# Kernel optimization log

Hardware: AMD Instinct MI355X
Metric: run time of the kernel (lower is better)

The kernel has to match this reference:

```python
import jax, jax.numpy as jnp
import numpy as np

VOCAB, EMBED, MAXLEN, UNITS, F1, BATCH = 50000, 256, 512, 32, 16, 512

def setup_inputs() -> dict:
    key = jax.random.key(0)
    ks = jax.random.split(key, 9)
    tokens = jax.random.randint(ks[0], (BATCH, MAXLEN), 0, VOCAB, dtype=jnp.int32)
    emb_table = jax.random.normal(ks[1], (VOCAB, EMBED), dtype=jnp.float32) * 0.02
    # SimpleRNN params (Keras: kernel, recurrent_kernel, bias)
    Wx = jax.random.normal(ks[2], (EMBED, UNITS), dtype=jnp.float32) * (1.0 / np.sqrt(EMBED))
    Wh = jax.random.normal(ks[3], (UNITS, UNITS), dtype=jnp.float32) * (1.0 / np.sqrt(UNITS))
    b  = jnp.zeros((UNITS,), dtype=jnp.float32)
    W1 = jax.random.normal(ks[4], (UNITS, F1), dtype=jnp.float32) * (1.0 / np.sqrt(UNITS))
    b1 = jnp.zeros((F1,), dtype=jnp.float32)
    W2 = jax.random.normal(ks[5], (F1, 1), dtype=jnp.float32) * (1.0 / np.sqrt(F1))
    b2 = jnp.zeros((1,), dtype=jnp.float32)
    return {"tokens": tokens, "emb_table": emb_table, "Wx": Wx, "Wh": Wh, "b": b,
            "W1": W1, "b1": b1, "W2": W2, "b2": b2}

def reference(tokens, emb_table, Wx, Wh, b, W1, b1, W2, b2):
    # Embedding lookup: [B, T, E]
    x = emb_table[tokens]
    # SimpleRNN recurrence (tanh), return last hidden state. Dropout disabled (inference).
    xs = jnp.transpose(x, (1, 0, 2))  # time-major [T, B, E]
    h0 = jnp.zeros((tokens.shape[0], Wh.shape[0]), dtype=x.dtype)

    def step(h, x_t):
        h_new = jnp.tanh(x_t @ Wx + h @ Wh + b)
        return h_new, None

    h_last, _ = jax.lax.scan(step, h0, xs)
    # Flatten is a no-op on [B, 32]; Dense heads are linear (no activation), then sigmoid.
    z = (h_last @ W1 + b1) @ W2 + b2
    return jax.nn.sigmoid(z)  # [B, 1]
```

## Files before the change

### kernel.cpp

```cpp
#include <hip/hip_runtime.h>
#include <hip/hip_bf16.h>
#include <math.h>

#define TT 512
#define BB 512
#define EE 256
#define UU 32
#define FF1 16
#define NWAVE 2048

#define TWO_LOG2E 2.8853900817779268f

__device__ __forceinline__ float rdlane(float v, int lane) {
    return __int_as_float(__builtin_amdgcn_readlane(__float_as_int(v), lane));
}

#define DPP_ADD(v, ctrl)                                                    \
    (v) += __int_as_float(__builtin_amdgcn_update_dpp(                      \
        0, __float_as_int(v), (ctrl), 0xf, 0xf, true))

__global__ __launch_bounds__(64) void proj_dpp(
    const float* __restrict__ emb, const float* __restrict__ Wx,
    const float* __restrict__ bias, float* __restrict__ P, int nrows)
{
    const int L = threadIdx.x;
    const int g = L >> 4;
    const int c = L & 15;
    const int wv = blockIdx.x;

    float w[16][8];
    #pragma unroll
    for (int kk = 0; kk < 16; ++kk) {
        const float4* src = (const float4*)(Wx + (size_t)(kk * 16 + c) * UU + g * 8);
        float4 a = src[0], b = src[1];
        w[kk][0] = a.x; w[kk][1] = a.y; w[kk][2] = a.z; w[kk][3] = a.w;
        w[kk][4] = b.x; w[kk][5] = b.y; w[kk][6] = b.z; w[kk][7] = b.w;
    }
    float bs[8];
    #pragma unroll
    for (int uu = 0; uu < 8; ++uu) bs[uu] = bias[g * 8 + uu];

    auto rowptr = [&](int i) {
        int r = wv + NWAVE * i;
        if (r >= nrows) r = nrows - 1;
        return emb + (size_t)r * EE;
    };

    float xA[16], xB[16];
    {
        const float* rp = rowptr(0);
        #pragma unroll
        for (int kk = 0; kk < 16; ++kk) xA[kk] = rp[kk * 16 + c];
    }

    const int NI = (nrows - 1 - wv) / NWAVE + 1;

    for (int i = 0; i < NI; ++i) {
        {
            const float* rp = rowptr(i + 1 < NI ? i + 1 : i);
            #pragma unroll
            for (int kk = 0; kk < 16; ++kk) xB[kk] = rp[kk * 16 + c];
        }

        float p[8];
        #pragma unroll
        for (int uu = 0; uu < 8; ++uu) p[uu] = 0.f;
        #pragma unroll
        for (int kk = 0; kk < 16; ++kk) {
            const float xk = xA[kk];
            #pragma unroll
            for (int uu = 0; uu < 8; ++uu)
                p[uu] = fmaf(xk, w[kk][uu], p[uu]);
        }

        #pragma unroll
        for (int uu = 0; uu < 8; ++uu) {
            DPP_ADD(p[uu], 0x111);
            DPP_ADD(p[uu], 0x112);
            DPP_ADD(p[uu], 0x114);
            DPP_ADD(p[uu], 0x118);
        }

        if (c == 15) {
            const int r = wv + NWAVE * i;
            float4 o0, o1;
            o0.x = (p[0] + bs[0]) * TWO_LOG2E;
            o0.y = (p[1] + bs[1]) * TWO_LOG2E;
            o0.z = (p[2] + bs[2]) * TWO_LOG2E;
            o0.w = (p[3] + bs[3]) * TWO_LOG2E;
            o1.x = (p[4] + bs[4]) * TWO_LOG2E;
            o1.y = (p[5] + bs[5]) * TWO_LOG2E;
            o1.z = (p[6] + bs[6]) * TWO_LOG2E;
            o1.w = (p[7] + bs[7]) * TWO_LOG2E;
            float4* dst = (float4*)(P + (size_t)r * UU + g * 8);
            dst[0] = o0; dst[1] = o1;
        }

        #pragma unroll
        for (int kk = 0; kk < 16; ++kk) xA[kk] = xB[kk];
    }
}

__global__ __launch_bounds__(64) void scan_heads(
    const int* __restrict__ tokens, const float* __restrict__ P,
    const float* __restrict__ Wh,
    const float* __restrict__ W1, const float* __restrict__ b1,
    const float* __restrict__ W2, const float* __restrict__ b2,
    float* __restrict__ out)
{
    __shared__ float xs[TT * UU];

    const int L = threadIdx.x;
    const int c = L & 15;
    const int u = c + ((L >> 5) << 4);
    const int b = blockIdx.x;
    const int* trow = tokens + b * TT;

    int probe = __builtin_amdgcn_update_dpp(0, c, 0x121, 0xf, 0xf, true);
    const int kstep = (__builtin_amdgcn_readfirstlane(probe) == 15) ? -1 : 1;

    float wA[16], wB[16];
    #pragma unroll
    for (int jj = 0; jj < 16; ++jj) {
        const int kj = (c + kstep * jj) & 15;
        wA[jj] = TWO_LOG2E * Wh[kj * UU + u];
        wB[jj] = TWO_LOG2E * Wh[(16 + kj) * UU + u];
    }

    const int sub = L >> 3;
    const int q   = L & 7;
    for (int cc = 0; cc < 8; ++cc) {
        int tk8[8];
        #pragma unroll
        for (int i = 0; i < 8; ++i)
            tk8[i] = trow[cc * 64 + i * 8 + sub];
        #pragma unroll
        for (int i = 0; i < 8; ++i) {
            const float* src = P + (size_t)tk8[i] * UU + q * 4;
            float* dst = xs + (cc * 64 + i * 8) * UU;
            __builtin_amdgcn_global_load_lds(
                (const __attribute__((address_space(1))) void*)src,
                (__attribute__((address_space(3))) void*)dst, 16, 0, 0);
        }
    }
    __syncthreads();

    float xr[8];
    #pragma unroll
    for (int j = 0; j < 8; ++j) xr[j] = xs[j * UU + u];

    float h = 0.f;

    for (int t = 0; t < TT; t += 8) {
        float xn[8];
        #pragma unroll
        for (int j = 0; j < 8; ++j)
            xn[j] = xs[((t + 8 + j) & (TT - 1)) * UU + u];

        #pragma unroll
        for (int j = 0; j < 8; ++j) {
            float A  = h;
            float Bv = h;
            asm("s_nop 1\n\t"
                "v_permlane32_swap_b32 %0, %1\n\t"
                "s_nop 1"
                : "+v"(A), "+v"(Bv));

            float a0, a1, a2, a3;
            asm("v_fma_f32  %0, %4, %6, %5\n\t"
                "v_mul_f32  %1, %4, %7  row_ror:1\n\t"
                "v_mul_f32  %2, %4, %8  row_ror:2\n\t"
                "v_mul_f32  %3, %4, %9  row_ror:3\n\t"
                "v_fmac_f32 %0, %4, %10 row_ror:4\n\t"
                "v_fmac_f32 %1, %4, %11 row_ror:5\n\t"
                "v_fmac_f32 %2, %4, %12 row_ror:6\n\t"
                "v_fmac_f32 %3, %4, %13 row_ror:7\n\t"
                "v_fmac_f32 %0, %4, %14 row_ror:8\n\t"
                "v_fmac_f32 %1, %4, %15 row_ror:9\n\t"
                "v_fmac_f32 %2, %4, %16 row_ror:10\n\t"
                "v_fmac_f32 %3, %4, %17 row_ror:11\n\t"
                "v_fmac_f32 %0, %4, %18 row_ror:12\n\t"
                "v_fmac_f32 %1, %4, %19 row_ror:13\n\t"
                "v_fmac_f32 %2, %4, %20 row_ror:14\n\t"
                "v_fmac_f32 %3, %4, %21 row_ror:15"
                : "=&v"(a0), "=&v"(a1), "=&v"(a2), "=&v"(a3)
                : "v"(A), "v"(xr[j]),
                  "v"(wA[0]),  "v"(wA[1]),  "v"(wA[2]),  "v"(wA[3]),
                  "v"(wA[4]),  "v"(wA[5]),  "v"(wA[6]),  "v"(wA[7]),
                  "v"(wA[8]),  "v"(wA[9]),  "v"(wA[10]), "v"(wA[11]),
                  "v"(wA[12]), "v"(wA[13]), "v"(wA[14]), "v"(wA[15]));

            asm("v_fmac_f32 %0, %4, %5\n\t"
                "v_fmac_f32 %1, %4, %6  row_ror:1\n\t"
                "v_fmac_f32 %2, %4, %7  row_ror:2\n\t"
                "v_fmac_f32 %3, %4, %8  row_ror:3\n\t"
                "v_fmac_f32 %0, %4, %9  row_ror:4\n\t"
                "v_fmac_f32 %1, %4, %10 row_ror:5\n\t"
                "v_fmac_f32 %2, %4, %11 row_ror:6\n\t"
                "v_fmac_f32 %3, %4, %12 row_ror:7\n\t"
                "v_fmac_f32 %0, %4, %13 row_ror:8\n\t"
                "v_fmac_f32 %1, %4, %14 row_ror:9\n\t"
                "v_fmac_f32 %2, %4, %15 row_ror:10\n\t"
                "v_fmac_f32 %3, %4, %16 row_ror:11\n\t"
                "v_fmac_f32 %0, %4, %17 row_ror:12\n\t"
                "v_fmac_f32 %1, %4, %18 row_ror:13\n\t"
                "v_fmac_f32 %2, %4, %19 row_ror:14\n\t"
                "v_fmac_f32 %3, %4, %20 row_ror:15"
                : "+v"(a0), "+v"(a1), "+v"(a2), "+v"(a3)
                : "v"(Bv),
                  "v"(wB[0]),  "v"(wB[1]),  "v"(wB[2]),  "v"(wB[3]),
                  "v"(wB[4]),  "v"(wB[5]),  "v"(wB[6]),  "v"(wB[7]),
                  "v"(wB[8]),  "v"(wB[9]),  "v"(wB[10]), "v"(wB[11]),
                  "v"(wB[12]), "v"(wB[13]), "v"(wB[14]), "v"(wB[15]));

            float e = __builtin_amdgcn_exp2f((a0 + a1) + (a2 + a3));
            float r = __builtin_amdgcn_rcpf(e + 1.0f);
            h = fmaf(-2.0f, r, 1.0f);
            xr[j] = xn[j];
        }
    }

    const int jh = L & 15;
    float s = b1[jh];
    #pragma unroll
    for (int k = 0; k < UU; ++k) {
        float hk = rdlane(h, (k & 15) + ((k >> 4) << 5));
        s = fmaf(hk, W1[k * FF1 + jh], s);
    }
    float z = b2[0];
    #pragma unroll
    for (int jj = 0; jj < FF1; ++jj) {
        float yj = rdlane(s, jj);
        z = fmaf(yj, W2[jj], z);
    }
    if (L == 0) {
        float e = __builtin_amdgcn_exp2f(-z * 1.4426950408889634f);
        out[b] = __builtin_amdgcn_rcpf(1.0f + e);
    }
}

extern "C" void kernel_launch(void* const* d_in, const int* in_sizes, int n_in,
                              void* d_out, int out_size, void* d_ws, size_t ws_size,
                              hipStream_t stream) {
    const int*   tokens = (const int*)  d_in[0];
    const float* emb    = (const float*)d_in[1];
    const float* Wx     = (const float*)d_in[2];
    const float* Wh     = (const float*)d_in[3];
    const float* bias   = (const float*)d_in[4];
    const float* W1     = (const float*)d_in[5];
    const float* b1     = (const float*)d_in[6];
    const float* W2     = (const float*)d_in[7];
    const float* b2     = (const float*)d_in[8];
    float* out = (float*)d_out;

    const int vocab = in_sizes[1] / EE;
    float* P = (float*)d_ws;

    proj_dpp<<<dim3(NWAVE), dim3(64), 0, stream>>>(
        emb, Wx, bias, P, vocab);

    scan_heads<<<dim3(BB), dim3(64), 0, stream>>>(
        tokens, P, Wh, W1, b1, W2, b2, out);
}
```

Before: 175.2 us.

## Split recurrent matvec across row halves and fold tanh affine into weights

The recurrence now carries r = 1/(1+e) instead of h and rewrites h = 1 - 2r. The constant term from Wh's column sums is folded into the projected bias, and -2 is folded into the recurrent weights, which removes the per-step fma. The 32-term dot product is split so that each 16-lane row handles half of k with 16 DPP fmas instead of 32. Partial sums are combined with a permlane16 swap. The serial chain per step gets shorter, at the cost of an extra cross-lane swap and a select, plus slightly different rounding.

```diff
diff --git a/kernel.cpp b/kernel.cpp
--- a/kernel.cpp
+++ b/kernel.cpp
@@ -21,7 +21,8 @@
 
 __global__ __launch_bounds__(64) void proj_dpp(
     const float* __restrict__ emb, const float* __restrict__ Wx,
-    const float* __restrict__ bias, float* __restrict__ P, int nrows)
+    const float* __restrict__ bias, const float* __restrict__ Wh,
+    float* __restrict__ P, int nrows)
 {
     const int L = threadIdx.x;
     const int g = L >> 4;
@@ -38,7 +39,12 @@
     }
     float bs[8];
     #pragma unroll
-    for (int uu = 0; uu < 8; ++uu) bs[uu] = bias[g * 8 + uu];
+    for (int uu = 0; uu < 8; ++uu) {
+        const int ucol = g * 8 + uu;
+        float s = 0.f;
+        for (int k = 0; k < UU; ++k) s += Wh[k * UU + ucol];
+        bs[uu] = 0.5f * TWO_LOG2E * (bias[ucol] + s);
+    }
 
     auto rowptr = [&](int i) {
         int r = wv + NWAVE * i;
@@ -83,15 +89,16 @@
 
         if (c == 15) {
             const int r = wv + NWAVE * i;
+            const float c0 = 0.5f * TWO_LOG2E;
             float4 o0, o1;
-            o0.x = (p[0] + bs[0]) * TWO_LOG2E;
-            o0.y = (p[1] + bs[1]) * TWO_LOG2E;
-            o0.z = (p[2] + bs[2]) * TWO_LOG2E;
-            o0.w = (p[3] + bs[3]) * TWO_LOG2E;
-            o1.x = (p[4] + bs[4]) * TWO_LOG2E;
-            o1.y = (p[5] + bs[5]) * TWO_LOG2E;
-            o1.z = (p[6] + bs[6]) * TWO_LOG2E;
-            o1.w = (p[7] + bs[7]) * TWO_LOG2E;
+            o0.x = fmaf(p[0], c0, bs[0]);
+            o0.y = fmaf(p[1], c0, bs[1]);
+            o0.z = fmaf(p[2], c0, bs[2]);
+            o0.w = fmaf(p[3], c0, bs[3]);
+            o1.x = fmaf(p[4], c0, bs[4]);
+            o1.y = fmaf(p[5], c0, bs[5]);
+            o1.z = fmaf(p[6], c0, bs[6]);
+            o1.w = fmaf(p[7], c0, bs[7]);
             float4* dst = (float4*)(P + (size_t)r * UU + g * 8);
             dst[0] = o0; dst[1] = o1;
         }
@@ -112,19 +119,20 @@
 
     const int L = threadIdx.x;
     const int c = L & 15;
+    const int khalf = ((L >> 4) & 1) << 4;
     const int u = c + ((L >> 5) << 4);
+    const bool oddrow = ((L >> 4) & 1) != 0;
     const int b = blockIdx.x;
     const int* trow = tokens + b * TT;
 
     int probe = __builtin_amdgcn_update_dpp(0, c, 0x121, 0xf, 0xf, true);
     const int kstep = (__builtin_amdgcn_readfirstlane(probe) == 15) ? -1 : 1;
 
-    float wA[16], wB[16];
+    float wr[16];
     #pragma unroll
     for (int jj = 0; jj < 16; ++jj) {
-        const int kj = (c + kstep * jj) & 15;
-        wA[jj] = TWO_LOG2E * Wh[kj * UU + u];
-        wB[jj] = TWO_LOG2E * Wh[(16 + kj) * UU + u];
+        const int kj = ((c + kstep * jj) & 15) + khalf;
+        wr[jj] = -2.0f * TWO_LOG2E * Wh[kj * UU + u];
     }
 
     const int sub = L >> 3;
@@ -149,7 +157,7 @@
     #pragma unroll
     for (int j = 0; j < 8; ++j) xr[j] = xs[j * UU + u];
 
-    float h = 0.f;
+    float r = 0.5f;
 
     for (int t = 0; t < TT; t += 8) {
         float xn[8];
@@ -159,15 +167,17 @@
 
         #pragma unroll
         for (int j = 0; j < 8; ++j) {
-            float A  = h;
-            float Bv = h;
+            float A  = r;
+            float Bv = r;
             asm("s_nop 1\n\t"
                 "v_permlane32_swap_b32 %0, %1\n\t"
                 "s_nop 1"
                 : "+v"(A), "+v"(Bv));
-
-            float a0, a1, a2, a3;
-            asm("v_fma_f32  %0, %4, %6, %5\n\t"
+            float H = oddrow ? Bv : A;
+
+            float p0, p1, p2, p3;
+            asm("s_nop 1\n\t"
+                "v_fma_f32  %0, %4, %6, %5\n\t"
                 "v_mul_f32  %1, %4, %7  row_ror:1\n\t"
                 "v_mul_f32  %2, %4, %8  row_ror:2\n\t"
                 "v_mul_f32  %3, %4, %9  row_ror:3\n\t"
@@ -183,42 +193,28 @@
                 "v_fmac_f32 %1, %4, %19 row_ror:13\n\t"
                 "v_fmac_f32 %2, %4, %20 row_ror:14\n\t"
                 "v_fmac_f32 %3, %4, %21 row_ror:15"
-                : "=&v"(a0), "=&v"(a1), "=&v"(a2), "=&v"(a3)
-                : "v"(A), "v"(xr[j]),
-                  "v"(wA[0]),  "v"(wA[1]),  "v"(wA[2]),  "v"(wA[3]),
-                  "v"(wA[4]),  "v"(wA[5]),  "v"(wA[6]),  "v"(wA[7]),
-                  "v"(wA[8]),  "v"(wA[9]),  "v"(wA[10]), "v"(wA[11]),
-                  "v"(wA[12]), "v"(wA[13]), "v"(wA[14]), "v"(wA[15]));
-
-            asm("v_fmac_f32 %0, %4, %5\n\t"
-                "v_fmac_f32 %1, %4, %6  row_ror:1\n\t"
-                "v_fmac_f32 %2, %4, %7  row_ror:2\n\t"
-                "v_fmac_f32 %3, %4, %8  row_ror:3\n\t"
-                "v_fmac_f32 %0, %4, %9  row_ror:4\n\t"
-                "v_fmac_f32 %1, %4, %10 row_ror:5\n\t"
-                "v_fmac_f32 %2, %4, %11 row_ror:6\n\t"
-                "v_fmac_f32 %3, %4, %12 row_ror:7\n\t"
-                "v_fmac_f32 %0, %4, %13 row_ror:8\n\t"
-                "v_fmac_f32 %1, %4, %14 row_ror:9\n\t"
-                "v_fmac_f32 %2, %4, %15 row_ror:10\n\t"
-                "v_fmac_f32 %3, %4, %16 row_ror:11\n\t"
-                "v_fmac_f32 %0, %4, %17 row_ror:12\n\t"
-                "v_fmac_f32 %1, %4, %18 row_ror:13\n\t"
-                "v_fmac_f32 %2, %4, %19 row_ror:14\n\t"
-                "v_fmac_f32 %3, %4, %20 row_ror:15"
-                : "+v"(a0), "+v"(a1), "+v"(a2), "+v"(a3)
-                : "v"(Bv),
-                  "v"(wB[0]),  "v"(wB[1]),  "v"(wB[2]),  "v"(wB[3]),
-                  "v"(wB[4]),  "v"(wB[5]),  "v"(wB[6]),  "v"(wB[7]),
-                  "v"(wB[8]),  "v"(wB[9]),  "v"(wB[10]), "v"(wB[11]),
-                  "v"(wB[12]), "v"(wB[13]), "v"(wB[14]), "v"(wB[15]));
-
-            float e = __builtin_amdgcn_exp2f((a0 + a1) + (a2 + a3));
-            float r = __builtin_amdgcn_rcpf(e + 1.0f);
-            h = fmaf(-2.0f, r, 1.0f);
+                : "=&v"(p0), "=&v"(p1), "=&v"(p2), "=&v"(p3)
+                : "v"(H), "v"(xr[j]),
+                  "v"(wr[0]),  "v"(wr[1]),  "v"(wr[2]),  "v"(wr[3]),
+                  "v"(wr[4]),  "v"(wr[5]),  "v"(wr[6]),  "v"(wr[7]),
+                  "v"(wr[8]),  "v"(wr[9]),  "v"(wr[10]), "v"(wr[11]),
+                  "v"(wr[12]), "v"(wr[13]), "v"(wr[14]), "v"(wr[15]));
+
+            float p = (p0 + p1) + (p2 + p3);
+
+            float pA = p, pB = p;
+            asm("s_nop 1\n\t"
+                "v_permlane16_swap_b32 %0, %1\n\t"
+                "s_nop 1"
+                : "+v"(pA), "+v"(pB));
+
+            float e = __builtin_amdgcn_exp2f(pA + pB);
+            r = __builtin_amdgcn_rcpf(e + 1.0f);
             xr[j] = xn[j];
         }
     }
+
+    float h = fmaf(-2.0f, r, 1.0f);
 
     const int jh = L & 15;
     float s = b1[jh];
@@ -257,7 +253,7 @@
     float* P = (float*)d_ws;
 
     proj_dpp<<<dim3(NWAVE), dim3(64), 0, stream>>>(
-        emb, Wx, bias, P, vocab);
+        emb, Wx, bias, Wh, P, vocab);
 
     scan_heads<<<dim3(BB), dim3(64), 0, stream>>>(
         tokens, P, Wh, W1, b1, W2, b2, out);
```

Result: slower. 187.6 us (+7.1%).
